# Kernel optimization log

Measured on AMD Instinct MI355X. Metric: run time of the kernel, lower is better.

The kernel has to match this reference:

```python
import jax, jax.numpy as jnp
import numpy as np

H = 16       # num_heads
FD = 16      # feature_dim
HD = 64      # head_dim = hidden // num_kv_heads
EPS = 1e-5   # attention normalization eps
LN_EPS = 1e-5


def setup_inputs() -> dict:
    key = jax.random.key(0)
    ks = jax.random.split(key, 5)
    b, l, hid = 2, 2048, 1024
    x = jax.random.normal(ks[0], (b, l, hid), dtype=jnp.float32)
    Wq = jax.random.normal(ks[1], (H * FD, hid), dtype=jnp.float32) * 0.02
    Wk = jax.random.normal(ks[2], (H * FD, hid), dtype=jnp.float32) * 0.02
    Wv = jax.random.normal(ks[3], (hid, hid), dtype=jnp.float32) * 0.02
    Wo = jax.random.normal(ks[4], (hid, hid), dtype=jnp.float32) * 0.02
    gamma = jnp.ones((FD,), dtype=jnp.float32)
    beta = jnp.zeros((FD,), dtype=jnp.float32)
    return {"x": x, "Wq": Wq, "Wk": Wk, "Wv": Wv, "Wo": Wo, "gamma": gamma, "beta": beta}


def _feature_map(t, gamma, beta):
    # RebasedFeatureMap without flatten: layer_norm (no affine) -> *gamma + beta
    mu = jnp.mean(t, axis=-1, keepdims=True)
    var = jnp.mean(jnp.square(t - mu), axis=-1, keepdims=True)
    t = (t - mu) * jax.lax.rsqrt(var + LN_EPS)
    return t * gamma + beta


def reference(x, Wq, Wk, Wv, Wo, gamma, beta):
    b, l, hid = x.shape
    # projections -> (b, h, l, d)
    q = (x @ Wq.T).reshape(b, l, H, FD).transpose(0, 2, 1, 3)
    k = (x @ Wk.T).reshape(b, l, H, FD).transpose(0, 2, 1, 3)
    v = (x @ Wv.T).reshape(b, l, H, HD).transpose(0, 2, 1, 3)
    q = _feature_map(q, gamma, beta) * (FD ** -0.5)  # use_scale=True in parallel_rebased
    k = _feature_map(k, gamma, beta)
    # phi(q).phi(k) with squared feature map == (q.k)^2
    s = jnp.square(jnp.einsum('bhid,bhjd->bhij', q, k))
    mask = jnp.tril(jnp.ones((l, l), dtype=bool))  # causal
    s = jnp.where(mask, s, jnp.float32(0))
    o = jnp.einsum('bhij,bhjd->bhid', s, v)
    z = jnp.sum(s, axis=-1, keepdims=True) + EPS    # use_normalize=True
    o = o / z
    o = o.transpose(0, 2, 1, 3).reshape(b, l, H * HD)
    return o @ Wo.T
```

## Files before the change

kernel.cpp:

```cpp
#include <hip/hip_runtime.h>
#include <cstddef>
#include <cstdint>


typedef __attribute__((ext_vector_type(8)))  __bf16 bf16x8;
typedef __attribute__((ext_vector_type(2)))  __bf16 bf16x2;
typedef __attribute__((ext_vector_type(4)))  float  f32x4;
typedef __attribute__((ext_vector_type(16))) float  f32x16;
typedef __attribute__((ext_vector_type(8)))  unsigned short ushort8;
typedef __attribute__((ext_vector_type(4)))  unsigned short ushort4v;
typedef __attribute__((ext_vector_type(4)))  unsigned int   uint4v;

__device__ __forceinline__ unsigned short f2b(float f) {
    union { float f; unsigned u; } v; v.f = f;
    unsigned r = v.u + 0x7FFFu + ((v.u >> 16) & 1u);
    return (unsigned short)(r >> 16);
}
__device__ __forceinline__ float b2f(unsigned short b) {
    union { unsigned u; float f; } v; v.u = ((unsigned)b) << 16;
    return v.f;
}
__device__ __forceinline__ unsigned pk2(float a, float b) {
    bf16x2 p; p[0] = (__bf16)a; p[1] = (__bf16)b;
    return __builtin_bit_cast(unsigned, p);
}

typedef const __attribute__((address_space(1))) void* gas_ptr;
typedef __attribute__((address_space(3))) void* las_ptr;

__device__ __forceinline__ void gload_lds16(const unsigned short* g, unsigned short* l) {
    __builtin_amdgcn_global_load_lds((gas_ptr)g, (las_ptr)l, 16, 0, 0);
}

template <int BM, int BN, int OUTMODE>
__global__ __launch_bounds__(256) void gemm_mfma(const unsigned short* __restrict__ A,
                                                 const unsigned short* __restrict__ W,
                                                 void* __restrict__ Cout,
                                                 int M, int N, int K) {
    constexpr int BK = 64;
    constexpr int MF = BM / 32;
    constexpr int NF = BN / 32;
    __shared__ __align__(16) unsigned short As[2][BM * BK];
    __shared__ __align__(16) unsigned short Bs[2][BN * BK];

    const int t = threadIdx.x;
    const int wid = t >> 6, lane = t & 63;
    const int m0 = blockIdx.x * BM, n0 = blockIdx.y * BN;
    const int wrow = (wid >> 1) * (BM / 2);
    const int wcol = (wid & 1) * (BN / 2);
    const int lr = lane & 15, lk = (lane >> 4) * 8;

    f32x4 acc[MF][NF];
#pragma unroll
    for (int m = 0; m < MF; ++m)
#pragma unroll
        for (int n = 0; n < NF; ++n) acc[m][n] = (f32x4){0.f, 0.f, 0.f, 0.f};

    const unsigned short* Ag = A + (size_t)m0 * K;
    const unsigned short* Wg = W + (size_t)n0 * K;

#define G_STAGE(k0_, buf_)                                                        \
    do {                                                                          \
        _Pragma("unroll")                                                         \
        for (int i = 0; i < BM / 32; ++i) {                                       \
            const int e = (i * 256 + wid * 64 + lane) * 8;                        \
            gload_lds16(Ag + (size_t)(e >> 6) * K + (k0_) + (e & 63),             \
                        &As[buf_][(size_t)(i * 256 + wid * 64) * 8]);             \
        }                                                                         \
        _Pragma("unroll")                                                         \
        for (int i = 0; i < BN / 32; ++i) {                                       \
            const int e = (i * 256 + wid * 64 + lane) * 8;                        \
            gload_lds16(Wg + (size_t)(e >> 6) * K + (k0_) + (e & 63),             \
                        &Bs[buf_][(size_t)(i * 256 + wid * 64) * 8]);             \
        }                                                                         \
    } while (0)

    const int nk = K / BK;
    G_STAGE(0, 0);
    __syncthreads();

    for (int ki = 0; ki < nk; ++ki) {
        const int cur = ki & 1;
        if (ki + 1 < nk) G_STAGE((ki + 1) * BK, cur ^ 1);

#pragma unroll
        for (int kk = 0; kk < BK; kk += 32) {
            bf16x8 af[MF], bf[NF];
#pragma unroll
            for (int m = 0; m < MF; ++m)
                af[m] = *(const bf16x8*)&As[cur][(wrow + m * 16 + lr) * BK + kk + lk];
#pragma unroll
            for (int n = 0; n < NF; ++n)
                bf[n] = *(const bf16x8*)&Bs[cur][(wcol + n * 16 + lr) * BK + kk + lk];
#pragma unroll
            for (int m = 0; m < MF; ++m)
#pragma unroll
                for (int n = 0; n < NF; ++n)
                    acc[m][n] = __builtin_amdgcn_mfma_f32_16x16x32_bf16(af[m], bf[n], acc[m][n], 0, 0, 0);
        }
        __syncthreads();
    }
#undef G_STAGE

    const int orow0 = m0 + wrow + (lane >> 4) * 4;
    const int ocol0 = n0 + wcol + lr;
#pragma unroll
    for (int m = 0; m < MF; ++m)
#pragma unroll
        for (int n = 0; n < NF; ++n) {
            if (OUTMODE == 2) {
                const int nc = ocol0 + n * 16;
                const int mrow = orow0 + m * 16;
                unsigned short* dst = (unsigned short*)Cout
                    + (size_t)((mrow >> 11) * 16 + (nc >> 6)) * (64 * 2048)
                    + (size_t)(nc & 63) * 2048 + (mrow & 2047);
                ushort4v pv;
#pragma unroll
                for (int i = 0; i < 4; ++i) pv[i] = f2b(acc[m][n][i]);
                *(ushort4v*)dst = pv;
            } else {
#pragma unroll
                for (int i = 0; i < 4; ++i) {
                    const size_t idx = (size_t)(orow0 + m * 16 + i) * N + ocol0 + n * 16;
                    if (OUTMODE == 1) ((unsigned short*)Cout)[idx] = f2b(acc[m][n][i]);
                    else              ((float*)Cout)[idx] = acc[m][n][i];
                }
            }
        }
}

__global__ __launch_bounds__(256) void gemm_split(const unsigned short* __restrict__ Ah,
                                                  const unsigned short* __restrict__ Al,
                                                  const unsigned short* __restrict__ Wh,
                                                  const unsigned short* __restrict__ Wl,
                                                  float* __restrict__ C,
                                                  int M, int N, int K) {
    constexpr int BM = 64, BN = 64, BK = 64;
    constexpr int MF = 2, NF = 2;
    __shared__ __align__(16) unsigned short Ahs[2][BM * BK];
    __shared__ __align__(16) unsigned short Als[2][BM * BK];
    __shared__ __align__(16) unsigned short Bhs[2][BN * BK];
    __shared__ __align__(16) unsigned short Bls[2][BN * BK];

    const int t = threadIdx.x;
    const int wid = t >> 6, lane = t & 63;
    const int m0 = blockIdx.x * BM, n0 = blockIdx.y * BN;
    const int wrow = (wid >> 1) * 32;
    const int wcol = (wid & 1) * 32;
    const int lr = lane & 15, lk = (lane >> 4) * 8;

    f32x4 acc[MF][NF];
#pragma unroll
    for (int m = 0; m < MF; ++m)
#pragma unroll
        for (int n = 0; n < NF; ++n) acc[m][n] = (f32x4){0.f, 0.f, 0.f, 0.f};

    const unsigned short* Ahg = Ah + (size_t)m0 * K;
    const unsigned short* Alg = Al + (size_t)m0 * K;
    const unsigned short* Whg = Wh + (size_t)n0 * K;
    const unsigned short* Wlg = Wl + (size_t)n0 * K;

#define S_STAGE(k0_, buf_)                                                        \
    do {                                                                          \
        _Pragma("unroll")                                                         \
        for (int i = 0; i < 2; ++i) {                                             \
            const int e = (i * 256 + wid * 64 + lane) * 8;                        \
            const size_t go = (size_t)(e >> 6) * K + (k0_) + (e & 63);            \
            const size_t lo = (size_t)(i * 256 + wid * 64) * 8;                   \
            gload_lds16(Ahg + go, &Ahs[buf_][lo]);                                \
            gload_lds16(Alg + go, &Als[buf_][lo]);                                \
            gload_lds16(Whg + go, &Bhs[buf_][lo]);                                \
            gload_lds16(Wlg + go, &Bls[buf_][lo]);                                \
        }                                                                         \
    } while (0)

    const int nk = K / BK;
    S_STAGE(0, 0);
    __syncthreads();

    for (int ki = 0; ki < nk; ++ki) {
        const int cur = ki & 1;
        if (ki + 1 < nk) S_STAGE((ki + 1) * BK, cur ^ 1);

#pragma unroll
        for (int kk = 0; kk < BK; kk += 32) {
            bf16x8 afh[MF], afl[MF], bfh[NF], bfl[NF];
#pragma unroll
            for (int m = 0; m < MF; ++m) {
                afh[m] = *(const bf16x8*)&Ahs[cur][(wrow + m * 16 + lr) * BK + kk + lk];
                afl[m] = *(const bf16x8*)&Als[cur][(wrow + m * 16 + lr) * BK + kk + lk];
            }
#pragma unroll
            for (int n = 0; n < NF; ++n) {
                bfh[n] = *(const bf16x8*)&Bhs[cur][(wcol + n * 16 + lr) * BK + kk + lk];
                bfl[n] = *(const bf16x8*)&Bls[cur][(wcol + n * 16 + lr) * BK + kk + lk];
            }
#pragma unroll
            for (int m = 0; m < MF; ++m)
#pragma unroll
                for (int n = 0; n < NF; ++n) {
                    acc[m][n] = __builtin_amdgcn_mfma_f32_16x16x32_bf16(afh[m], bfh[n], acc[m][n], 0, 0, 0);
                    acc[m][n] = __builtin_amdgcn_mfma_f32_16x16x32_bf16(afh[m], bfl[n], acc[m][n], 0, 0, 0);
                    acc[m][n] = __builtin_amdgcn_mfma_f32_16x16x32_bf16(afl[m], bfh[n], acc[m][n], 0, 0, 0);
                }
        }
        __syncthreads();
    }
#undef S_STAGE

    const int orow0 = m0 + wrow + (lane >> 4) * 4;
    const int ocol0 = n0 + wcol + lr;
#pragma unroll
    for (int m = 0; m < MF; ++m)
#pragma unroll
        for (int n = 0; n < NF; ++n)
#pragma unroll
            for (int i = 0; i < 4; ++i)
                C[(size_t)(orow0 + m * 16 + i) * N + ocol0 + n * 16] = acc[m][n][i];
}

__global__ __launch_bounds__(256) void cast_bf16(const float* __restrict__ in,
                                                 unsigned short* __restrict__ out, int n) {
    const int i = (blockIdx.x * 256 + threadIdx.x) * 8;
    if (i >= n) return;
    float4 a = *(const float4*)(in + i);
    float4 b = *(const float4*)(in + i + 4);
    ushort8 o;
    o[0] = f2b(a.x); o[1] = f2b(a.y); o[2] = f2b(a.z); o[3] = f2b(a.w);
    o[4] = f2b(b.x); o[5] = f2b(b.y); o[6] = f2b(b.z); o[7] = f2b(b.w);
    *(ushort8*)(out + i) = o;
}

__global__ __launch_bounds__(256) void cast_split(const float* __restrict__ in,
                                                  unsigned short* __restrict__ hi,
                                                  unsigned short* __restrict__ lo, int n) {
    const int i = (blockIdx.x * 256 + threadIdx.x) * 8;
    if (i >= n) return;
    float4 a = *(const float4*)(in + i);
    float4 b = *(const float4*)(in + i + 4);
    float xv[8] = {a.x, a.y, a.z, a.w, b.x, b.y, b.z, b.w};
    ushort8 oh, ol;
#pragma unroll
    for (int e = 0; e < 8; ++e) {
        const unsigned short h = f2b(xv[e]);
        oh[e] = h;
        ol[e] = f2b(xv[e] - b2f(h));
    }
    *(ushort8*)(hi + i) = oh;
    *(ushort8*)(lo + i) = ol;
}

__global__ __launch_bounds__(256) void ln_featuremap(const float* __restrict__ qk,
                                                     const float* __restrict__ gamma,
                                                     const float* __restrict__ beta,
                                                     unsigned short* __restrict__ qhl,
                                                     unsigned short* __restrict__ khl) {
    const int gid = blockIdx.x * 256 + threadIdx.x;
    const int idx = gid & 31;
    const int m = gid >> 5;
    const int b = m >> 11, l = m & 2047;
    const int h = idx & 15;
    const float scale = (idx < 16) ? 0.25f : 1.0f;
    const float* p = qk + (size_t)gid * 16;

    float xv[16];
    float4 v0 = *(const float4*)(p + 0);
    float4 v1 = *(const float4*)(p + 4);
    float4 v2 = *(const float4*)(p + 8);
    float4 v3 = *(const float4*)(p + 12);
    xv[0]=v0.x; xv[1]=v0.y; xv[2]=v0.z; xv[3]=v0.w;
    xv[4]=v1.x; xv[5]=v1.y; xv[6]=v1.z; xv[7]=v1.w;
    xv[8]=v2.x; xv[9]=v2.y; xv[10]=v2.z; xv[11]=v2.w;
    xv[12]=v3.x; xv[13]=v3.y; xv[14]=v3.z; xv[15]=v3.w;

    float mu = 0.f;
#pragma unroll
    for (int f = 0; f < 16; ++f) mu += xv[f];
    mu *= 0.0625f;
    float var = 0.f;
#pragma unroll
    for (int f = 0; f < 16; ++f) { float d = xv[f] - mu; var = fmaf(d, d, var); }
    var *= 0.0625f;
    const float rs = rsqrtf(var + 1e-5f);

    ushort8 hi0, hi1, lo0, lo1;
#pragma unroll
    for (int f = 0; f < 16; ++f) {
        const float v = ((xv[f] - mu) * rs * gamma[f] + beta[f]) * scale;
        const unsigned short hb = f2b(v);
        const unsigned short lb = f2b(v - b2f(hb));
        if (f < 8) { hi0[f] = hb; lo0[f] = lb; }
        else       { hi1[f - 8] = hb; lo1[f - 8] = lb; }
    }
    unsigned short* dst = ((idx < 16) ? qhl : khl)
        + ((size_t)(b * 16 + h) * 2048 + l) * 32;
    *(ushort8*)(dst + 0)  = hi0;
    *(ushort8*)(dst + 8)  = hi1;
    *(ushort8*)(dst + 16) = lo0;
    *(ushort8*)(dst + 24) = lo1;
}

__global__ __launch_bounds__(512) void rebased_attn(const unsigned short* __restrict__ qhl_g,
                                                    const unsigned short* __restrict__ khl_g,
                                                    const unsigned short* __restrict__ vT,
                                                    unsigned short* __restrict__ o) {
    const int bh = blockIdx.x;
    const int x  = blockIdx.y;
    const int bb = bh >> 4;
    const int t = threadIdx.x;
    const int wid = t >> 6, lane = t & 63;
    const int lq = lane & 31, lh = lane >> 5;
    const int tq = wid >> 1, qs = wid & 1;
    const int qt = (tq == 0) ? x : (tq == 1) ? (15 - x) : (tq == 2) ? (16 + x) : (31 - x);
    const int qtmax = 31 - x;

    __shared__ __align__(16) unsigned short khl[3][4 * 64 * 8];
    __shared__ __align__(16) unsigned short vsl[3][8 * 64 * 8];
    __shared__ float zbuf[8][32];

    const unsigned short* qg  = qhl_g + (size_t)bh * 2048 * 32;
    const unsigned short* kg  = khl_g + (size_t)bh * 2048 * 32;
    const unsigned short* vbh = vT + (size_t)bh * 64 * 2048;
    unsigned short*       obh = o  + (size_t)bb * 2048 * 1024 + (bh & 15) * 64;

    const f32x16 zc16 = (f32x16)(0.f);

    const unsigned short* qr_ = qg + (size_t)(qt * 64 + qs * 32 + lq) * 32;
    const bf16x8 bqh = *(const bf16x8*)&qr_[lh * 8];
    const bf16x8 bql = *(const bf16x8*)&qr_[16 + lh * 8];

#define STAGE_KV(kt_, buf_)                                                            \
    do {                                                                               \
        if (wid < 4)                                                                   \
            gload_lds16(kg + ((size_t)((kt_) << 6) + lane) * 32 + wid * 8,             \
                        &khl[buf_][wid * 512]);                                        \
        gload_lds16(vbh + (size_t)lane * 2048 + ((kt_) << 6) + wid * 8,                \
                    &vsl[buf_][wid * 512]);                                            \
    } while (0)

    STAGE_KV(0, 0);
    STAGE_KV(1, 1);
    if (wid < 4) asm volatile("s_waitcnt vmcnt(2)" ::: "memory");
    else         asm volatile("s_waitcnt vmcnt(1)" ::: "memory");
    __builtin_amdgcn_s_barrier();

    f32x16 oacc[2];
    oacc[0] = zc16; oacc[1] = zc16;
    float zl = 0.f;

    for (int kt = 0; kt <= qtmax; ++kt) {
        const int cur = kt % 3;
        const bool pf = (kt + 2 <= qtmax);
        if (pf) STAGE_KV(kt + 2, (kt + 2) % 3);

        if (kt <= qt) {
            __builtin_amdgcn_s_setprio(1);
            f32x16 D[2];
#pragma unroll
            for (int st = 0; st < 2; ++st) {
                const bf16x8 kh = *(const bf16x8*)&khl[cur][((lh    ) * 64 + st * 32 + lq) * 8];
                const bf16x8 kl = *(const bf16x8*)&khl[cur][((2 + lh) * 64 + st * 32 + lq) * 8];
                f32x16 a = __builtin_amdgcn_mfma_f32_32x32x16_bf16(kh, bql, zc16, 0, 0, 0);
                a = __builtin_amdgcn_mfma_f32_32x32x16_bf16(kl, bqh, a, 0, 0, 0);
                a = __builtin_amdgcn_mfma_f32_32x32x16_bf16(kh, bqh, a, 0, 0, 0);
                D[st] = a;
            }
            const bool diag = (kt == qt);
#pragma unroll
            for (int st = 0; st < 2; ++st)
#pragma unroll
                for (int r = 0; r < 16; ++r) {
                    const float v = D[st][r];
                    float s2 = v * v;
                    if (diag) {
                        const int kr = st * 32 + (r & 3) + 8 * (r >> 2) + 4 * lh;
                        s2 = (kr <= qs * 32 + lq) ? s2 : 0.f;
                    }
                    zl += s2;
                    D[st][r] = s2;
                }
#pragma unroll
            for (int ks = 0; ks < 4; ++ks) {
                const int st = ks >> 1, b = 8 * (ks & 1);
                const bf16x8 vb0 = *(const bf16x8*)&vsl[cur][((2 * ks + lh) * 64 + 0 * 32 + lq) * 8];
                const bf16x8 vb1 = *(const bf16x8*)&vsl[cur][((2 * ks + lh) * 64 + 1 * 32 + lq) * 8];
                unsigned u0 = pk2(D[st][b + 0], D[st][b + 1]);
                unsigned u1 = pk2(D[st][b + 2], D[st][b + 3]);
                unsigned v0 = pk2(D[st][b + 4], D[st][b + 5]);
                unsigned v1 = pk2(D[st][b + 6], D[st][b + 7]);
                asm("v_permlane32_swap_b32 %0, %1" : "+v"(u0), "+v"(v0));
                asm("v_permlane32_swap_b32 %0, %1" : "+v"(u1), "+v"(v1));
                uint4v pw; pw[0] = u0; pw[1] = u1; pw[2] = v0; pw[3] = v1;
                const bf16x8 pa = __builtin_bit_cast(bf16x8, pw);
                oacc[0] = __builtin_amdgcn_mfma_f32_32x32x16_bf16(pa, vb0, oacc[0], 0, 0, 0);
                oacc[1] = __builtin_amdgcn_mfma_f32_32x32x16_bf16(pa, vb1, oacc[1], 0, 0, 0);
            }
            __builtin_amdgcn_s_setprio(0);
        }

        if (pf) {
            if (wid < 4) asm volatile("s_waitcnt vmcnt(2)" ::: "memory");
            else         asm volatile("s_waitcnt vmcnt(1)" ::: "memory");
        } else {
            asm volatile("s_waitcnt vmcnt(0)" ::: "memory");
        }
        __builtin_amdgcn_s_barrier();
    }
#undef STAGE_KV

    {
        const float z = zl + __shfl_xor(zl, 32);
        if (lh == 0) zbuf[wid][lq] = 1.f / (z + 1e-5f);
    }
#pragma unroll
    for (int dt = 0; dt < 2; ++dt)
#pragma unroll
        for (int r = 0; r < 16; ++r) {
            const int qr = (r & 3) + 8 * (r >> 2) + 4 * lh;
            const float zi = zbuf[wid][qr];
            obh[(size_t)(qt * 64 + qs * 32 + qr) * 1024 + dt * 32 + lq] =
                f2b(oacc[dt][r] * zi);
        }
}

extern "C" void kernel_launch(void* const* d_in, const int* in_sizes, int n_in,
                              void* d_out, int out_size, void* d_ws, size_t ws_size,
                              hipStream_t stream) {
    const float* x     = (const float*)d_in[0];
    const float* Wq    = (const float*)d_in[1];
    const float* Wk    = (const float*)d_in[2];
    const float* Wv    = (const float*)d_in[3];
    const float* Wo    = (const float*)d_in[4];
    const float* gamma = (const float*)d_in[5];
    const float* beta  = (const float*)d_in[6];
    float* out = (float*)d_out;
    (void)in_sizes; (void)n_in; (void)out_size; (void)ws_size;

    char* w = (char*)d_ws;
    float*          qk_raw = (float*)w;
    unsigned short* vTb    = (unsigned short*)(w + (8u  << 20));
    unsigned short* ob     = (unsigned short*)(w + (16u << 20));
    unsigned short* xh     = (unsigned short*)(w + (24u << 20));
    unsigned short* xl     = (unsigned short*)(w + (32u << 20));
    unsigned short* qhl_g  = (unsigned short*)(w + (24u << 20));
    unsigned short* khl_g  = (unsigned short*)(w + (28u << 20));
    unsigned short* wqkh   = (unsigned short*)(w + (40u << 20));
    unsigned short* wqkl   = (unsigned short*)(w + (41u << 20));
    unsigned short* wvb    = (unsigned short*)(w + (42u << 20));
    unsigned short* wob    = (unsigned short*)(w + (44u << 20));

    cast_split<<<2048, 256, 0, stream>>>(x,  xh, xl, 4096 * 1024);
    cast_split<<<128,  256, 0, stream>>>(Wq, wqkh, wqkl, 256 * 1024);
    cast_split<<<128,  256, 0, stream>>>(Wk, wqkh + 256 * 1024, wqkl + 256 * 1024, 256 * 1024);
    cast_bf16 <<<512,  256, 0, stream>>>(Wv, wvb, 1024 * 1024);
    cast_bf16 <<<512,  256, 0, stream>>>(Wo, wob, 1024 * 1024);

    gemm_split<<<dim3(64, 8), 256, 0, stream>>>(xh, xl, wqkh, wqkl, qk_raw, 4096, 512, 1024);
    gemm_mfma<128, 64, 2><<<dim3(32, 16), 256, 0, stream>>>(xh, wvb, vTb, 4096, 1024, 1024);
    ln_featuremap<<<512, 256, 0, stream>>>(qk_raw, gamma, beta, qhl_g, khl_g);
    rebased_attn<<<dim3(32, 8), 512, 0, stream>>>(qhl_g, khl_g, vTb, ob);
    gemm_mfma<128, 64, 0><<<dim3(32, 16), 256, 0, stream>>>(ob, wob, out, 4096, 1024, 1024);
}
```

Before: 119.7 us.

## Fuse LayerNorm feature map into QK split GEMM epilogue and merge cast kernels

The layer-norm feature map is now computed in the QK projection GEMM epilogue, using 16-lane shuffle reductions over each head's 16 features. The result is written straight to the hi/lo bf16 Q/K layout, so the fp32 qk_raw round trip and a separate kernel launch go away. The weight cast kernels are also merged pairwise, cutting launches from five to three. Risks: the variance uses the E[x^2]-mu^2 form, which is less numerically stable, and the scattered 2-byte epilogue stores may be poorly coalesced.

New measurement: 116.5 us. -2.7%, faster.

```diff
diff --git a/kernel.cpp b/kernel.cpp
--- a/kernel.cpp
+++ b/kernel.cpp
@@ -129,12 +129,15 @@
         }
 }
 
-__global__ __launch_bounds__(256) void gemm_split(const unsigned short* __restrict__ Ah,
-                                                  const unsigned short* __restrict__ Al,
-                                                  const unsigned short* __restrict__ Wh,
-                                                  const unsigned short* __restrict__ Wl,
-                                                  float* __restrict__ C,
-                                                  int M, int N, int K) {
+__global__ __launch_bounds__(256) void gemm_split_ln(const unsigned short* __restrict__ Ah,
+                                                     const unsigned short* __restrict__ Al,
+                                                     const unsigned short* __restrict__ Wh,
+                                                     const unsigned short* __restrict__ Wl,
+                                                     const float* __restrict__ gamma,
+                                                     const float* __restrict__ beta,
+                                                     unsigned short* __restrict__ qhl,
+                                                     unsigned short* __restrict__ khl,
+                                                     int M, int N, int K) {
     constexpr int BM = 64, BN = 64, BK = 64;
     constexpr int MF = 2, NF = 2;
     __shared__ __align__(16) unsigned short Ahs[2][BM * BK];
@@ -209,26 +212,55 @@
 #undef S_STAGE
 
     const int orow0 = m0 + wrow + (lane >> 4) * 4;
-    const int ocol0 = n0 + wcol + lr;
-#pragma unroll
-    for (int m = 0; m < MF; ++m)
-#pragma unroll
-        for (int n = 0; n < NF; ++n)
-#pragma unroll
-            for (int i = 0; i < 4; ++i)
-                C[(size_t)(orow0 + m * 16 + i) * N + ocol0 + n * 16] = acc[m][n][i];
-}
-
-__global__ __launch_bounds__(256) void cast_bf16(const float* __restrict__ in,
-                                                 unsigned short* __restrict__ out, int n) {
+    const float gl = gamma[lr];
+    const float bl = beta[lr];
+#pragma unroll
+    for (int n = 0; n < NF; ++n) {
+        const int head_all = (n0 + wcol + n * 16) >> 4;
+        const float scale = (head_all < 16) ? 0.25f : 1.0f;
+        unsigned short* base = (head_all < 16) ? qhl : khl;
+        const size_t hoff = (size_t)(head_all & 15) * (2048 * 32);
+#pragma unroll
+        for (int m = 0; m < MF; ++m)
+#pragma unroll
+            for (int i = 0; i < 4; ++i) {
+                const float v = acc[m][n][i];
+                float s = v, sq = v * v;
+#pragma unroll
+                for (int msk = 1; msk < 16; msk <<= 1) {
+                    s  += __shfl_xor(s,  msk);
+                    sq += __shfl_xor(sq, msk);
+                }
+                const float mu  = s * 0.0625f;
+                const float var = sq * 0.0625f - mu * mu;
+                const float rs  = rsqrtf(var + 1e-5f);
+                const float val = ((v - mu) * rs * gl + bl) * scale;
+                const unsigned short hb = f2b(val);
+                const unsigned short lb = f2b(val - b2f(hb));
+                const int mrow = orow0 + m * 16 + i;
+                const int bb = mrow >> 11, l = mrow & 2047;
+                unsigned short* dst = base + (size_t)bb * (16 * 2048 * 32) + hoff + (size_t)l * 32;
+                dst[lr]      = hb;
+                dst[16 + lr] = lb;
+            }
+    }
+}
+
+__global__ __launch_bounds__(256) void cast_bf16_2(const float* __restrict__ a,
+                                                   const float* __restrict__ b,
+                                                   unsigned short* __restrict__ oa,
+                                                   unsigned short* __restrict__ ob_,
+                                                   int na) {
     const int i = (blockIdx.x * 256 + threadIdx.x) * 8;
-    if (i >= n) return;
-    float4 a = *(const float4*)(in + i);
-    float4 b = *(const float4*)(in + i + 4);
+    const float* in = (i < na) ? a : b;
+    unsigned short* out = (i < na) ? oa : ob_;
+    const int j = (i < na) ? i : (i - na);
+    float4 p = *(const float4*)(in + j);
+    float4 q = *(const float4*)(in + j + 4);
     ushort8 o;
-    o[0] = f2b(a.x); o[1] = f2b(a.y); o[2] = f2b(a.z); o[3] = f2b(a.w);
-    o[4] = f2b(b.x); o[5] = f2b(b.y); o[6] = f2b(b.z); o[7] = f2b(b.w);
-    *(ushort8*)(out + i) = o;
+    o[0] = f2b(p.x); o[1] = f2b(p.y); o[2] = f2b(p.z); o[3] = f2b(p.w);
+    o[4] = f2b(q.x); o[5] = f2b(q.y); o[6] = f2b(q.z); o[7] = f2b(q.w);
+    *(ushort8*)(out + j) = o;
 }
 
 __global__ __launch_bounds__(256) void cast_split(const float* __restrict__ in,
@@ -250,54 +282,26 @@
     *(ushort8*)(lo + i) = ol;
 }
 
-__global__ __launch_bounds__(256) void ln_featuremap(const float* __restrict__ qk,
-                                                     const float* __restrict__ gamma,
-                                                     const float* __restrict__ beta,
-                                                     unsigned short* __restrict__ qhl,
-                                                     unsigned short* __restrict__ khl) {
-    const int gid = blockIdx.x * 256 + threadIdx.x;
-    const int idx = gid & 31;
-    const int m = gid >> 5;
-    const int b = m >> 11, l = m & 2047;
-    const int h = idx & 15;
-    const float scale = (idx < 16) ? 0.25f : 1.0f;
-    const float* p = qk + (size_t)gid * 16;
-
-    float xv[16];
-    float4 v0 = *(const float4*)(p + 0);
-    float4 v1 = *(const float4*)(p + 4);
-    float4 v2 = *(const float4*)(p + 8);
-    float4 v3 = *(const float4*)(p + 12);
-    xv[0]=v0.x; xv[1]=v0.y; xv[2]=v0.z; xv[3]=v0.w;
-    xv[4]=v1.x; xv[5]=v1.y; xv[6]=v1.z; xv[7]=v1.w;
-    xv[8]=v2.x; xv[9]=v2.y; xv[10]=v2.z; xv[11]=v2.w;
-    xv[12]=v3.x; xv[13]=v3.y; xv[14]=v3.z; xv[15]=v3.w;
-
-    float mu = 0.f;
-#pragma unroll
-    for (int f = 0; f < 16; ++f) mu += xv[f];
-    mu *= 0.0625f;
-    float var = 0.f;
-#pragma unroll
-    for (int f = 0; f < 16; ++f) { float d = xv[f] - mu; var = fmaf(d, d, var); }
-    var *= 0.0625f;
-    const float rs = rsqrtf(var + 1e-5f);
-
-    ushort8 hi0, hi1, lo0, lo1;
-#pragma unroll
-    for (int f = 0; f < 16; ++f) {
-        const float v = ((xv[f] - mu) * rs * gamma[f] + beta[f]) * scale;
-        const unsigned short hb = f2b(v);
-        const unsigned short lb = f2b(v - b2f(hb));
-        if (f < 8) { hi0[f] = hb; lo0[f] = lb; }
-        else       { hi1[f - 8] = hb; lo1[f - 8] = lb; }
-    }
-    unsigned short* dst = ((idx < 16) ? qhl : khl)
-        + ((size_t)(b * 16 + h) * 2048 + l) * 32;
-    *(ushort8*)(dst + 0)  = hi0;
-    *(ushort8*)(dst + 8)  = hi1;
-    *(ushort8*)(dst + 16) = lo0;
-    *(ushort8*)(dst + 24) = lo1;
+__global__ __launch_bounds__(256) void cast_split2(const float* __restrict__ a,
+                                                   const float* __restrict__ b,
+                                                   unsigned short* __restrict__ hi,
+                                                   unsigned short* __restrict__ lo,
+                                                   int na) {
+    const int i = (blockIdx.x * 256 + threadIdx.x) * 8;
+    const float* in = (i < na) ? a : b;
+    const int j = (i < na) ? i : (i - na);
+    float4 p = *(const float4*)(in + j);
+    float4 q = *(const float4*)(in + j + 4);
+    float xv[8] = {p.x, p.y, p.z, p.w, q.x, q.y, q.z, q.w};
+    ushort8 oh, ol;
+#pragma unroll
+    for (int e = 0; e < 8; ++e) {
+        const unsigned short h = f2b(xv[e]);
+        oh[e] = h;
+        ol[e] = f2b(xv[e] - b2f(h));
+    }
+    *(ushort8*)(hi + i) = oh;
+    *(ushort8*)(lo + i) = ol;
 }
 
 __global__ __launch_bounds__(512) void rebased_attn(const unsigned short* __restrict__ qhl_g,
@@ -437,27 +441,25 @@
     (void)in_sizes; (void)n_in; (void)out_size; (void)ws_size;
 
     char* w = (char*)d_ws;
-    float*          qk_raw = (float*)w;
     unsigned short* vTb    = (unsigned short*)(w + (8u  << 20));
     unsigned short* ob     = (unsigned short*)(w + (16u << 20));
     unsigned short* xh     = (unsigned short*)(w + (24u << 20));
     unsigned short* xl     = (unsigned short*)(w + (32u << 20));
-    unsigned short* qhl_g  = (unsigned short*)(w + (24u << 20));
-    unsigned short* khl_g  = (unsigned short*)(w + (28u << 20));
+    unsigned short* qhl_g  = (unsigned short*)(w + (0u  << 20));
+    unsigned short* khl_g  = (unsigned short*)(w + (4u  << 20));
     unsigned short* wqkh   = (unsigned short*)(w + (40u << 20));
     unsigned short* wqkl   = (unsigned short*)(w + (41u << 20));
     unsigned short* wvb    = (unsigned short*)(w + (42u << 20));
     unsigned short* wob    = (unsigned short*)(w + (44u << 20));
 
-    cast_split<<<2048, 256, 0, stream>>>(x,  xh, xl, 4096 * 1024);
-    cast_split<<<128,  256, 0, stream>>>(Wq, wqkh, wqkl, 256 * 1024);
-    cast_split<<<128,  256, 0, stream>>>(Wk, wqkh + 256 * 1024, wqkl + 256 * 1024, 256 * 1024);
-    cast_bf16 <<<512,  256, 0, stream>>>(Wv, wvb, 1024 * 1024);
-    cast_bf16 <<<512,  256, 0, stream>>>(Wo, wob, 1024 * 1024);
-
-    gemm_split<<<dim3(64, 8), 256, 0, stream>>>(xh, xl, wqkh, wqkl, qk_raw, 4096, 512, 1024);
+    cast_split<<<2048, 256, 0, stream>>>(x, xh, xl, 4096 * 1024);
+    cast_split2<<<256, 256, 0, stream>>>(Wq, Wk, wqkh, wqkl, 256 * 1024);
+    cast_bf16_2<<<1024, 256, 0, stream>>>(Wv, Wo, wvb, wob, 1024 * 1024);
+
+    gemm_split_ln<<<dim3(64, 8), 256, 0, stream>>>(xh, xl, wqkh, wqkl,
+                                                   gamma, beta, qhl_g, khl_g,
+                                                   4096, 512, 1024);
     gemm_mfma<128, 64, 2><<<dim3(32, 16), 256, 0, stream>>>(xh, wvb, vTb, 4096, 1024, 1024);
-    ln_featuremap<<<512, 256, 0, stream>>>(qk_raw, gamma, beta, qhl_g, khl_g);
     rebased_attn<<<dim3(32, 8), 512, 0, stream>>>(qhl_g, khl_g, vTb, ob);
     gemm_mfma<128, 64, 0><<<dim3(32, 16), 256, 0, stream>>>(ob, wob, out, 4096, 1024, 1024);
 }
```
